# Kernel optimization log

Measured on AMD Instinct MI355X. Metric: run time of the kernel, lower is better.

Reference implementation:

```python
import jax, jax.numpy as jnp
import numpy as np

N_NODES = 10000
N_EDGES = 320000
D = 256
D_OUT = 256
NUM_REL = 2


def setup_inputs() -> dict:
    key = jax.random.key(0)
    ks = jax.random.split(key, 16)
    s = 1.0 / np.sqrt(D)
    inp = {}
    inp['feat'] = jax.random.normal(ks[0], (N_NODES, D), dtype=jnp.float32)
    inp['src'] = jax.random.randint(ks[1], (N_EDGES,), 0, N_NODES, dtype=jnp.int32)
    inp['dst'] = jax.random.randint(ks[2], (N_EDGES,), 0, N_NODES, dtype=jnp.int32)
    inp['rel'] = jax.random.randint(ks[3], (N_EDGES,), 0, NUM_REL, dtype=jnp.int32)
    # per-relation edgeNN: ONE tied Linear(D, D) applied twice with relu
    inp['W_rel'] = jax.random.normal(ks[4], (NUM_REL, D, D), dtype=jnp.float32) * s
    inp['b_rel'] = jax.random.normal(ks[5], (NUM_REL, D), dtype=jnp.float32) * s
    # LSTM (single step from zero state: W_hh contributes 0, omitted)
    inp['W_ih'] = jax.random.normal(ks[6], (4 * D, D), dtype=jnp.float32) * s
    inp['b_ih'] = jax.random.normal(ks[7], (4 * D,), dtype=jnp.float32) * s
    inp['b_hh'] = jax.random.normal(ks[8], (4 * D,), dtype=jnp.float32) * s
    # global_update MLP: D -> D/2 -> D/2 -> D_OUT
    h = D // 2
    inp['W1'] = jax.random.normal(ks[9], (h, D), dtype=jnp.float32) * s
    inp['b1'] = jax.random.normal(ks[10], (h,), dtype=jnp.float32) * s
    inp['W2'] = jax.random.normal(ks[11], (h, h), dtype=jnp.float32) * (1.0 / np.sqrt(h))
    inp['b2'] = jax.random.normal(ks[12], (h,), dtype=jnp.float32) * (1.0 / np.sqrt(h))
    inp['W3'] = jax.random.normal(ks[13], (D_OUT, h), dtype=jnp.float32) * (1.0 / np.sqrt(h))
    inp['b3'] = jax.random.normal(ks[14], (D_OUT,), dtype=jnp.float32) * (1.0 / np.sqrt(h))
    return inp


def reference(feat, src, dst, rel, W_rel, b_rel, W_ih, b_ih, b_hh,
              W1, b1, W2, b2, W3, b3):
    n_nodes = feat.shape[0]
    # ---- message: per-edge relation-typed tied-weight MLP ----
    S = feat[src]  # [E, D] gather of source features

    def edge_nn(x, W, b):
        h = jax.nn.relu(x @ W.T + b)
        return jax.nn.relu(h @ W.T + b)  # same lin1 applied twice (tied)

    msgs = jnp.zeros_like(S)
    for r in range(W_rel.shape[0]):  # small fixed relation count
        msgs = jnp.where((rel == r)[:, None], edge_nn(S, W_rel[r], b_rel[r]), msgs)

    # ---- reduce: scatter-sum into destination nodes ----
    agg = jax.ops.segment_sum(msgs, dst, num_segments=n_nodes)  # [N, D]

    # ---- apply: per-node single-step LSTM from zero (h0, c0) ----
    gates = agg @ W_ih.T + b_ih + b_hh  # [N, 4D], torch gate order i,f,g,o
    i, f, g, o = jnp.split(gates, 4, axis=-1)
    c = jax.nn.sigmoid(i) * jnp.tanh(g)  # f * c0 = 0
    hn = jax.nn.sigmoid(o) * jnp.tanh(c)  # [N, D]

    # ---- global_update MLP ----
    x = jax.nn.relu(hn @ W1.T + b1)
    x = jax.nn.relu(x @ W2.T + b2)
    return x @ W3.T + b3  # [N, D_OUT]
```

## Files before the change

kernel.cpp:

```cpp
#include <hip/hip_runtime.h>
#include <hip/hip_bf16.h>

#define N_NODES 10000
#define N_EDGES 320000
#define D 256

typedef __attribute__((ext_vector_type(8))) _Float16 f16x8;
typedef __attribute__((ext_vector_type(4))) _Float16 f16x4;
typedef __attribute__((ext_vector_type(4))) float f32x4;

__device__ __forceinline__ void async_copy16(const void* g, void* l) {
  __builtin_amdgcn_global_load_lds(
      (const __attribute__((address_space(1))) unsigned int*)g,
      (__attribute__((address_space(3))) unsigned int*)l, 16, 0, 0);
}

template<int ROWS, int WAVES>
__device__ __forceinline__ void stage_tile(const _Float16* __restrict__ Wb, int k0, int K,
                                           _Float16* Bs, int wave, int lane) {
  const int sr = lane >> 2, ss = lane & 3;
#pragma unroll
  for (int grp = wave; grp < ROWS / 16; grp += WAVES) {
    int r = grp * 16 + sr;
    int gq = ss ^ ((r >> 1) & 3);
    async_copy16(Wb + (size_t)r * K + k0 + gq * 8, Bs + grp * 512);
  }
}
__device__ __forceinline__ f16x8 read_B(const _Float16* Bs, int r, int quad) {
  return *(const f16x8*)(Bs + r * 32 + (quad ^ ((r >> 1) & 3)) * 8);
}

__device__ __forceinline__ float fast_sigmoid(float x) {
  return __builtin_amdgcn_rcpf(1.f + __expf(-x));
}
__device__ __forceinline__ float fast_tanh(float x) {
  float ax = fabsf(x);
  float e = __expf(-2.f * ax);
  float t = (1.f - e) * __builtin_amdgcn_rcpf(1.f + e);
  return copysignf(t, x);
}

__global__ void prep_fill(const int* __restrict__ dst, const int* __restrict__ src,
                          const int* __restrict__ rel,
                          int* __restrict__ cnt, unsigned int* __restrict__ rowoff,
                          const float* __restrict__ W_rel, const float* __restrict__ W_ih,
                          const float* __restrict__ b_ih, const float* __restrict__ b_hh,
                          const float* __restrict__ W1, const float* __restrict__ W2,
                          const float* __restrict__ W3,
                          _Float16* __restrict__ W_relh, _Float16* __restrict__ Wg,
                          float* __restrict__ bg,
                          _Float16* __restrict__ W1h, _Float16* __restrict__ W2h,
                          _Float16* __restrict__ W3h) {
  int i = blockIdx.x * 256 + threadIdx.x;
  if (i < N_EDGES) {
    int v = dst[i];
    int pos = atomicAdd(&cnt[v], 1);
    if (pos < 128)
      rowoff[(v << 7) + pos] = (unsigned int)((rel[i] * N_NODES + src[i]) * D);
    return;
  }
  i -= N_EDGES;
  if (i < 131072) { W_relh[i] = (_Float16)W_rel[i]; return; }
  i -= 131072;
  if (i < 196608) {
    int p = i >> 8, k = i & 255;
    int t = p / 48, rem = p - t * 48;
    int phase = rem >> 4, u = rem & 15;
    int orig = t * 16 + u + (phase == 1 ? 512 : (phase == 2 ? 768 : 0));
    Wg[i] = (_Float16)W_ih[orig * 256 + k]; return;
  }
  i -= 196608;
  if (i < 32768) { W1h[i] = (_Float16)W1[i]; return; }
  i -= 32768;
  if (i < 16384) { W2h[i] = (_Float16)W2[i]; return; }
  i -= 16384;
  if (i < 32768) { W3h[i] = (_Float16)W3[i]; return; }
  i -= 32768;
  if (i < 768) {
    int t = i / 48, rem = i - t * 48;
    int phase = rem >> 4, u = rem & 15;
    int orig = t * 16 + u + (phase == 1 ? 512 : (phase == 2 ? 768 : 0));
    bg[i] = b_ih[orig] + b_hh[orig];
  }
}

__global__ __launch_bounds__(512) void edge_fused(
    const float* __restrict__ feat, const _Float16* __restrict__ W_relh,
    const float* __restrict__ b_rel, _Float16* __restrict__ Mh)
{
  __shared__ _Float16 Hs[64 * 266];
  __shared__ alignas(16) _Float16 Bs[256 * 32];
  const int t = threadIdx.x;
  const int wave = t >> 6, lane = t & 63;
  const int quad = lane >> 4, lrow = lane & 15;
  const int z = blockIdx.y;
  const int m0 = blockIdx.x * 64;
  const _Float16* Wb = W_relh + z * 65536;
  const float* bb = b_rel + z * 256;
  const int wm = (wave >> 2) * 32;
  const int wn = (wave & 3) * 64;

  int ar0 = m0 + wm + lrow;      if (ar0 > N_NODES - 1) ar0 = N_NODES - 1;
  int ar1 = m0 + wm + 16 + lrow; if (ar1 > N_NODES - 1) ar1 = N_NODES - 1;
  const float* fr0 = feat + (size_t)ar0 * 256;
  const float* fr1 = feat + (size_t)ar1 * 256;

  f32x4 acc[2][4];
#pragma unroll
  for (int i = 0; i < 2; ++i)
#pragma unroll
    for (int j = 0; j < 4; ++j) acc[i][j] = (f32x4)0.0f;

#pragma unroll
  for (int kc = 0; kc < 8; ++kc) {
    stage_tile<256, 8>(Wb, kc * 32, 256, Bs, wave, lane);
    float4 u0 = *(const float4*)(fr0 + kc * 32 + quad * 8);
    float4 u1 = *(const float4*)(fr0 + kc * 32 + quad * 8 + 4);
    float4 v0 = *(const float4*)(fr1 + kc * 32 + quad * 8);
    float4 v1 = *(const float4*)(fr1 + kc * 32 + quad * 8 + 4);
    f16x8 af0, af1;
    af0[0] = (_Float16)u0.x; af0[1] = (_Float16)u0.y; af0[2] = (_Float16)u0.z; af0[3] = (_Float16)u0.w;
    af0[4] = (_Float16)u1.x; af0[5] = (_Float16)u1.y; af0[6] = (_Float16)u1.z; af0[7] = (_Float16)u1.w;
    af1[0] = (_Float16)v0.x; af1[1] = (_Float16)v0.y; af1[2] = (_Float16)v0.z; af1[3] = (_Float16)v0.w;
    af1[4] = (_Float16)v1.x; af1[5] = (_Float16)v1.y; af1[6] = (_Float16)v1.z; af1[7] = (_Float16)v1.w;
    __syncthreads();
#pragma unroll
    for (int j = 0; j < 4; ++j) {
      f16x8 bf = read_B(Bs, wn + j * 16 + lrow, quad);
      acc[0][j] = __builtin_amdgcn_mfma_f32_16x16x32_f16(af0, bf, acc[0][j], 0, 0, 0);
      acc[1][j] = __builtin_amdgcn_mfma_f32_16x16x32_f16(af1, bf, acc[1][j], 0, 0, 0);
    }
    __syncthreads();
  }
#pragma unroll
  for (int i = 0; i < 2; ++i) {
    int rb = wm + i * 16 + quad * 4;
#pragma unroll
    for (int j = 0; j < 4; ++j) {
      int col = wn + j * 16 + lrow;
      float bv = bb[col];
#pragma unroll
      for (int reg = 0; reg < 4; ++reg) {
        Hs[(rb + reg) * 266 + col] = (_Float16)fmaxf(acc[i][j][reg] + bv, 0.f);
        acc[i][j][reg] = 0.f;
      }
    }
  }
  __syncthreads();

#pragma unroll
  for (int kc = 0; kc < 8; ++kc) {
    stage_tile<256, 8>(Wb, kc * 32, 256, Bs, wave, lane);
    f16x8 af0 = *(const f16x8*)(Hs + (wm + lrow) * 266 + kc * 32 + quad * 8);
    f16x8 af1 = *(const f16x8*)(Hs + (wm + 16 + lrow) * 266 + kc * 32 + quad * 8);
    __syncthreads();
#pragma unroll
    for (int j = 0; j < 4; ++j) {
      f16x8 bf = read_B(Bs, wn + j * 16 + lrow, quad);
      acc[0][j] = __builtin_amdgcn_mfma_f32_16x16x32_f16(af0, bf, acc[0][j], 0, 0, 0);
      acc[1][j] = __builtin_amdgcn_mfma_f32_16x16x32_f16(af1, bf, acc[1][j], 0, 0, 0);
    }
    __syncthreads();
  }
  _Float16* Mo = Mh + (size_t)z * (N_NODES * D);
#pragma unroll
  for (int i = 0; i < 2; ++i) {
    int rb = m0 + wm + i * 16 + quad * 4;
#pragma unroll
    for (int j = 0; j < 4; ++j) {
      int col = wn + j * 16 + lrow;
      float bv = bb[col];
#pragma unroll
      for (int reg = 0; reg < 4; ++reg) {
        int gm = rb + reg;
        if (gm < N_NODES)
          Mo[(size_t)gm * D + col] = (_Float16)fmaxf(acc[i][j][reg] + bv, 0.f);
      }
    }
  }
}

__global__ __launch_bounds__(256) void agg_kernel(const int* __restrict__ cnt,
                                                  const unsigned int* __restrict__ rowoff,
                                                  const _Float16* __restrict__ Mh,
                                                  _Float16* __restrict__ aggh) {
  __shared__ float part[4][256];
  const int node = blockIdx.x;
  const int wave = threadIdx.x >> 6, lane = threadIdx.x & 63;
  const int base = node << 7;
  const int deg = cnt[node];
  float a0 = 0.f, a1 = 0.f, a2 = 0.f, a3 = 0.f;
  for (int j = wave; j < deg; j += 4) {
    unsigned int off = rowoff[base + j];
    f16x4 v = *(const f16x4*)(Mh + (size_t)off + lane * 4);
    a0 += (float)v[0]; a1 += (float)v[1]; a2 += (float)v[2]; a3 += (float)v[3];
  }
  *(float4*)&part[wave][lane * 4] = make_float4(a0, a1, a2, a3);
  __syncthreads();
  if (wave == 0) {
    float4 p0 = *(const float4*)&part[0][lane * 4];
    float4 p1 = *(const float4*)&part[1][lane * 4];
    float4 p2 = *(const float4*)&part[2][lane * 4];
    float4 p3 = *(const float4*)&part[3][lane * 4];
    f16x4 o;
    o[0] = (_Float16)(p0.x + p1.x + p2.x + p3.x);
    o[1] = (_Float16)(p0.y + p1.y + p2.y + p3.y);
    o[2] = (_Float16)(p0.z + p1.z + p2.z + p3.z);
    o[3] = (_Float16)(p0.w + p1.w + p2.w + p3.w);
    *(f16x4*)(aggh + (size_t)node * D + lane * 4) = o;
  }
}

__global__ __launch_bounds__(256) void tail(
    const _Float16* __restrict__ aggh,
    const _Float16* __restrict__ Wg, const float* __restrict__ bg,
    const _Float16* __restrict__ W1h, const float* __restrict__ b1,
    const _Float16* __restrict__ W2h, const float* __restrict__ b2,
    const _Float16* __restrict__ W3h, const float* __restrict__ b3,
    float* __restrict__ out)
{
  __shared__ alignas(16) _Float16 Ws[768 * 32];
  __shared__ _Float16 Hn[16 * 266];
  __shared__ _Float16 Xs[16 * 138];
  __shared__ _Float16 X2s[16 * 138];
  const int t = threadIdx.x;
  const int wave = t >> 6, lane = t & 63;
  const int quad = lane >> 4, lrow = lane & 15;
  const int r0 = blockIdx.x * 16;

  {
    f16x8 af[8];
#pragma unroll
    for (int kc = 0; kc < 8; ++kc)
      af[kc] = *(const f16x8*)(aggh + (size_t)(r0 + lrow) * 256 + kc * 32 + quad * 8);
    f32x4 acc[12];
#pragma unroll
    for (int j = 0; j < 12; ++j) acc[j] = (f32x4)0.0f;
#pragma unroll
    for (int kc = 0; kc < 8; ++kc) {
      stage_tile<768, 4>(Wg, kc * 32, 256, Ws, wave, lane);
      __syncthreads();
#pragma unroll
      for (int j = 0; j < 12; ++j) {
        f16x8 bf = read_B(Ws, (wave * 12 + j) * 16 + lrow, quad);
        acc[j] = __builtin_amdgcn_mfma_f32_16x16x32_f16(af[kc], bf, acc[j], 0, 0, 0);
      }
      __syncthreads();
    }
#pragma unroll
    for (int p = 0; p < 4; ++p) {
      float bvi = bg[(wave * 12 + 3 * p + 0) * 16 + lrow];
      float bvg = bg[(wave * 12 + 3 * p + 1) * 16 + lrow];
      float bvo = bg[(wave * 12 + 3 * p + 2) * 16 + lrow];
      int dcol = (wave * 4 + p) * 16 + lrow;
#pragma unroll
      for (int reg = 0; reg < 4; ++reg) {
        float vi = acc[3 * p + 0][reg] + bvi;
        float vg = acc[3 * p + 1][reg] + bvg;
        float vo = acc[3 * p + 2][reg] + bvo;
        float c = fast_sigmoid(vi) * fast_tanh(vg);
        Hn[(quad * 4 + reg) * 266 + dcol] = (_Float16)(fast_sigmoid(vo) * fast_tanh(c));
      }
    }
  }
  __syncthreads();

  {
    f16x8 af[8];
#pragma unroll
    for (int kc = 0; kc < 8; ++kc)
      af[kc] = *(const f16x8*)(Hn + lrow * 266 + kc * 32 + quad * 8);
    f32x4 acc[2];
    acc[0] = (f32x4)0.0f; acc[1] = (f32x4)0.0f;
#pragma unroll
    for (int kc = 0; kc < 8; ++kc) {
      stage_tile<128, 4>(W1h, kc * 32, 256, Ws, wave, lane);
      __syncthreads();
#pragma unroll
      for (int j = 0; j < 2; ++j) {
        f16x8 bf = read_B(Ws, wave * 32 + j * 16 + lrow, quad);
        acc[j] = __builtin_amdgcn_mfma_f32_16x16x32_f16(af[kc], bf, acc[j], 0, 0, 0);
      }
      __syncthreads();
    }
#pragma unroll
    for (int j = 0; j < 2; ++j) {
      int col = wave * 32 + j * 16 + lrow;
      float bv = b1[col];
#pragma unroll
      for (int reg = 0; reg < 4; ++reg)
        Xs[(quad * 4 + reg) * 138 + col] = (_Float16)fmaxf(acc[j][reg] + bv, 0.f);
    }
  }
  __syncthreads();

  {
    f16x8 af[4];
#pragma unroll
    for (int kc = 0; kc < 4; ++kc)
      af[kc] = *(const f16x8*)(Xs + lrow * 138 + kc * 32 + quad * 8);
    f32x4 acc[2];
    acc[0] = (f32x4)0.0f; acc[1] = (f32x4)0.0f;
#pragma unroll
    for (int kc = 0; kc < 4; ++kc) {
      stage_tile<128, 4>(W2h, kc * 32, 128, Ws, wave, lane);
      __syncthreads();
#pragma unroll
      for (int j = 0; j < 2; ++j) {
        f16x8 bf = read_B(Ws, wave * 32 + j * 16 + lrow, quad);
        acc[j] = __builtin_amdgcn_mfma_f32_16x16x32_f16(af[kc], bf, acc[j], 0, 0, 0);
      }
      __syncthreads();
    }
#pragma unroll
    for (int j = 0; j < 2; ++j) {
      int col = wave * 32 + j * 16 + lrow;
      float bv = b2[col];
#pragma unroll
      for (int reg = 0; reg < 4; ++reg)
        X2s[(quad * 4 + reg) * 138 + col] = (_Float16)fmaxf(acc[j][reg] + bv, 0.f);
    }
  }
  __syncthreads();

  {
    f16x8 af[4];
#pragma unroll
    for (int kc = 0; kc < 4; ++kc)
      af[kc] = *(const f16x8*)(X2s + lrow * 138 + kc * 32 + quad * 8);
    f32x4 acc[4];
#pragma unroll
    for (int j = 0; j < 4; ++j) acc[j] = (f32x4)0.0f;
#pragma unroll
    for (int kc = 0; kc < 4; ++kc) {
      stage_tile<256, 4>(W3h, kc * 32, 128, Ws, wave, lane);
      __syncthreads();
#pragma unroll
      for (int j = 0; j < 4; ++j) {
        f16x8 bf = read_B(Ws, wave * 64 + j * 16 + lrow, quad);
        acc[j] = __builtin_amdgcn_mfma_f32_16x16x32_f16(af[kc], bf, acc[j], 0, 0, 0);
      }
      __syncthreads();
    }
#pragma unroll
    for (int j = 0; j < 4; ++j) {
      int col = wave * 64 + j * 16 + lrow;
      float bv = b3[col];
#pragma unroll
      for (int reg = 0; reg < 4; ++reg)
        out[(size_t)(r0 + quad * 4 + reg) * 256 + col] = acc[j][reg] + bv;
    }
  }
}

extern "C" void kernel_launch(void* const* d_in, const int* in_sizes, int n_in,
                              void* d_out, int out_size, void* d_ws, size_t ws_size,
                              hipStream_t stream) {
  const float* feat  = (const float*)d_in[0];
  const int* src = (const int*)d_in[1];
  const int* dst = (const int*)d_in[2];
  const int* rel = (const int*)d_in[3];
  const float* W_rel = (const float*)d_in[4];
  const float* b_rel = (const float*)d_in[5];
  const float* W_ih  = (const float*)d_in[6];
  const float* b_ih  = (const float*)d_in[7];
  const float* b_hh  = (const float*)d_in[8];
  const float* W1 = (const float*)d_in[9];
  const float* b1 = (const float*)d_in[10];
  const float* W2 = (const float*)d_in[11];
  const float* b2 = (const float*)d_in[12];
  const float* W3 = (const float*)d_in[13];
  const float* b3 = (const float*)d_in[14];
  float* out = (float*)d_out;

  char* ws = (char*)d_ws;
  _Float16* Mh   = (_Float16*)(ws);
  _Float16* aggh = (_Float16*)(ws + 10240000);
  char* wsb = ws + 15360000;
  _Float16* W_relh = (_Float16*)(wsb);
  _Float16* Wg     = (_Float16*)(wsb + 262144);
  _Float16* W1h    = (_Float16*)(wsb + 655360);
  _Float16* W2h    = (_Float16*)(wsb + 720896);
  _Float16* W3h    = (_Float16*)(wsb + 753664);
  float*    bg     = (float*)(wsb + 819200);
  int*      cnt    = (int*)(wsb + 822272);
  unsigned int* rowoff = (unsigned int*)(wsb + 862272);

  (void)hipMemsetAsync(cnt, 0, N_NODES * sizeof(int), stream);
  prep_fill<<<2853, 256, 0, stream>>>(dst, src, rel, cnt, rowoff,
                                      W_rel, W_ih, b_ih, b_hh, W1, W2, W3,
                                      W_relh, Wg, bg, W1h, W2h, W3h);
  edge_fused<<<dim3(157, 2), 512, 0, stream>>>(feat, W_relh, b_rel, Mh);
  agg_kernel<<<N_NODES, 256, 0, stream>>>(cnt, rowoff, Mh, aggh);
  tail<<<625, 256, 0, stream>>>(aggh, Wg, bg, W1h, b1, W2h, b2, W3h, b3, out);
}
```

Measured before the change: 210.9 us.

## Fuse prep work into edge kernel and stage fp32 relation weights directly

```diff
diff --git a/kernel.cpp b/kernel.cpp
--- a/kernel.cpp
+++ b/kernel.cpp
@@ -28,6 +28,23 @@
 }
 __device__ __forceinline__ f16x8 read_B(const _Float16* Bs, int r, int quad) {
   return *(const f16x8*)(Bs + r * 32 + (quad ^ ((r >> 1) & 3)) * 8);
+}
+
+__device__ __forceinline__ void stage_W_f32(const float* __restrict__ Wz, int k0,
+                                            _Float16* Bs, int t) {
+#pragma unroll
+  for (int rep = 0; rep < 2; ++rep) {
+    int slot = t + rep * 512;
+    int r = slot >> 2, q = slot & 3;
+    int gq = q ^ ((r >> 1) & 3);
+    const float* gp = Wz + r * 256 + k0 + gq * 8;
+    float4 a = *(const float4*)gp;
+    float4 b = *(const float4*)(gp + 4);
+    f16x8 h;
+    h[0] = (_Float16)a.x; h[1] = (_Float16)a.y; h[2] = (_Float16)a.z; h[3] = (_Float16)a.w;
+    h[4] = (_Float16)b.x; h[5] = (_Float16)b.y; h[6] = (_Float16)b.z; h[7] = (_Float16)b.w;
+    *(f16x8*)(Bs + r * 32 + q * 8) = h;
+  }
 }
 
 __device__ __forceinline__ float fast_sigmoid(float x) {
@@ -40,53 +57,16 @@
   return copysignf(t, x);
 }
 
-__global__ void prep_fill(const int* __restrict__ dst, const int* __restrict__ src,
-                          const int* __restrict__ rel,
-                          int* __restrict__ cnt, unsigned int* __restrict__ rowoff,
-                          const float* __restrict__ W_rel, const float* __restrict__ W_ih,
-                          const float* __restrict__ b_ih, const float* __restrict__ b_hh,
-                          const float* __restrict__ W1, const float* __restrict__ W2,
-                          const float* __restrict__ W3,
-                          _Float16* __restrict__ W_relh, _Float16* __restrict__ Wg,
-                          float* __restrict__ bg,
-                          _Float16* __restrict__ W1h, _Float16* __restrict__ W2h,
-                          _Float16* __restrict__ W3h) {
-  int i = blockIdx.x * 256 + threadIdx.x;
-  if (i < N_EDGES) {
-    int v = dst[i];
-    int pos = atomicAdd(&cnt[v], 1);
-    if (pos < 128)
-      rowoff[(v << 7) + pos] = (unsigned int)((rel[i] * N_NODES + src[i]) * D);
-    return;
-  }
-  i -= N_EDGES;
-  if (i < 131072) { W_relh[i] = (_Float16)W_rel[i]; return; }
-  i -= 131072;
-  if (i < 196608) {
-    int p = i >> 8, k = i & 255;
-    int t = p / 48, rem = p - t * 48;
-    int phase = rem >> 4, u = rem & 15;
-    int orig = t * 16 + u + (phase == 1 ? 512 : (phase == 2 ? 768 : 0));
-    Wg[i] = (_Float16)W_ih[orig * 256 + k]; return;
-  }
-  i -= 196608;
-  if (i < 32768) { W1h[i] = (_Float16)W1[i]; return; }
-  i -= 32768;
-  if (i < 16384) { W2h[i] = (_Float16)W2[i]; return; }
-  i -= 16384;
-  if (i < 32768) { W3h[i] = (_Float16)W3[i]; return; }
-  i -= 32768;
-  if (i < 768) {
-    int t = i / 48, rem = i - t * 48;
-    int phase = rem >> 4, u = rem & 15;
-    int orig = t * 16 + u + (phase == 1 ? 512 : (phase == 2 ? 768 : 0));
-    bg[i] = b_ih[orig] + b_hh[orig];
-  }
-}
-
 __global__ __launch_bounds__(512) void edge_fused(
-    const float* __restrict__ feat, const _Float16* __restrict__ W_relh,
-    const float* __restrict__ b_rel, _Float16* __restrict__ Mh)
+    const float* __restrict__ feat, const float* __restrict__ W_rel,
+    const float* __restrict__ b_rel, _Float16* __restrict__ Mh,
+    const int* __restrict__ dst, const int* __restrict__ src, const int* __restrict__ rel,
+    int* __restrict__ cnt, unsigned int* __restrict__ rowoff,
+    const float* __restrict__ W_ih, const float* __restrict__ b_ih,
+    const float* __restrict__ b_hh, const float* __restrict__ W1,
+    const float* __restrict__ W2, const float* __restrict__ W3,
+    _Float16* __restrict__ Wg, float* __restrict__ bg,
+    _Float16* __restrict__ W1h, _Float16* __restrict__ W2h, _Float16* __restrict__ W3h)
 {
   __shared__ _Float16 Hs[64 * 266];
   __shared__ alignas(16) _Float16 Bs[256 * 32];
@@ -95,10 +75,46 @@
   const int quad = lane >> 4, lrow = lane & 15;
   const int z = blockIdx.y;
   const int m0 = blockIdx.x * 64;
-  const _Float16* Wb = W_relh + z * 65536;
+  const float* Wz = W_rel + z * 65536;
   const float* bb = b_rel + z * 256;
   const int wm = (wave >> 2) * 32;
   const int wn = (wave & 3) * 64;
+
+  {
+    const int gtid = (blockIdx.y * gridDim.x + blockIdx.x) * 512 + t;
+#pragma unroll
+    for (int rep = 0; rep < 2; ++rep) {
+      int e = gtid + rep * 160768;
+      if (e < N_EDGES) {
+        int v = dst[e];
+        int pos = atomicAdd(&cnt[v], 1);
+        if (pos < 128)
+          rowoff[(v << 7) + pos] = (unsigned int)((rel[e] * N_NODES + src[e]) * D);
+      }
+      int i = gtid + rep * 160768;
+      if (i < 279296) {
+        if (i < 196608) {
+          int p = i >> 8, k = i & 255;
+          int tg = p / 48, rem = p - tg * 48;
+          int phase = rem >> 4, u = rem & 15;
+          int orig = tg * 16 + u + (phase == 1 ? 512 : (phase == 2 ? 768 : 0));
+          Wg[i] = (_Float16)W_ih[orig * 256 + k];
+        } else {
+          int j = i - 196608;
+          if (j < 32768) { W1h[j] = (_Float16)W1[j]; }
+          else if ((j -= 32768) < 16384) { W2h[j] = (_Float16)W2[j]; }
+          else if ((j -= 16384) < 32768) { W3h[j] = (_Float16)W3[j]; }
+          else {
+            int b = j - 32768;
+            int tg = b / 48, rem = b - tg * 48;
+            int phase = rem >> 4, u = rem & 15;
+            int orig = tg * 16 + u + (phase == 1 ? 512 : (phase == 2 ? 768 : 0));
+            bg[b] = b_ih[orig] + b_hh[orig];
+          }
+        }
+      }
+    }
+  }
 
   int ar0 = m0 + wm + lrow;      if (ar0 > N_NODES - 1) ar0 = N_NODES - 1;
   int ar1 = m0 + wm + 16 + lrow; if (ar1 > N_NODES - 1) ar1 = N_NODES - 1;
@@ -113,7 +129,7 @@
 
 #pragma unroll
   for (int kc = 0; kc < 8; ++kc) {
-    stage_tile<256, 8>(Wb, kc * 32, 256, Bs, wave, lane);
+    stage_W_f32(Wz, kc * 32, Bs, t);
     float4 u0 = *(const float4*)(fr0 + kc * 32 + quad * 8);
     float4 u1 = *(const float4*)(fr0 + kc * 32 + quad * 8 + 4);
     float4 v0 = *(const float4*)(fr1 + kc * 32 + quad * 8);
@@ -150,7 +166,7 @@
 
 #pragma unroll
   for (int kc = 0; kc < 8; ++kc) {
-    stage_tile<256, 8>(Wb, kc * 32, 256, Bs, wave, lane);
+    stage_W_f32(Wz, kc * 32, Bs, t);
     f16x8 af0 = *(const f16x8*)(Hs + (wm + lrow) * 266 + kc * 32 + quad * 8);
     f16x8 af1 = *(const f16x8*)(Hs + (wm + 16 + lrow) * 266 + kc * 32 + quad * 8);
     __syncthreads();
@@ -377,20 +393,18 @@
   _Float16* Mh   = (_Float16*)(ws);
   _Float16* aggh = (_Float16*)(ws + 10240000);
   char* wsb = ws + 15360000;
-  _Float16* W_relh = (_Float16*)(wsb);
-  _Float16* Wg     = (_Float16*)(wsb + 262144);
-  _Float16* W1h    = (_Float16*)(wsb + 655360);
-  _Float16* W2h    = (_Float16*)(wsb + 720896);
-  _Float16* W3h    = (_Float16*)(wsb + 753664);
-  float*    bg     = (float*)(wsb + 819200);
-  int*      cnt    = (int*)(wsb + 822272);
-  unsigned int* rowoff = (unsigned int*)(wsb + 862272);
+  _Float16* Wg  = (_Float16*)(wsb);
+  _Float16* W1h = (_Float16*)(wsb + 393216);
+  _Float16* W2h = (_Float16*)(wsb + 458752);
+  _Float16* W3h = (_Float16*)(wsb + 491520);
+  float*    bg  = (float*)(wsb + 557056);
+  int*      cnt = (int*)(wsb + 560128);
+  unsigned int* rowoff = (unsigned int*)(wsb + 600128);
 
   (void)hipMemsetAsync(cnt, 0, N_NODES * sizeof(int), stream);
-  prep_fill<<<2853, 256, 0, stream>>>(dst, src, rel, cnt, rowoff,
-                                      W_rel, W_ih, b_ih, b_hh, W1, W2, W3,
-                                      W_relh, Wg, bg, W1h, W2h, W3h);
-  edge_fused<<<dim3(157, 2), 512, 0, stream>>>(feat, W_relh, b_rel, Mh);
+  edge_fused<<<dim3(157, 2), 512, 0, stream>>>(
+      feat, W_rel, b_rel, Mh, dst, src, rel, cnt, rowoff,
+      W_ih, b_ih, b_hh, W1, W2, W3, Wg, bg, W1h, W2h, W3h);
   agg_kernel<<<N_NODES, 256, 0, stream>>>(cnt, rowoff, Mh, aggh);
   tail<<<625, 256, 0, stream>>>(aggh, Wg, bg, W1h, b1, W2h, b2, W3h, b3, out);
 }
```

Result: slower. 231.4 us (+9.7%).
